# Performance work log

Hardware: AMD Instinct MI355X
Metric: run time of the kernel (lower is better)

## Reference

```python
import jax, jax.numpy as jnp
import numpy as np

N_NODES = 50000
N_EDGES = 1600000
F_IN = 256
HID = 256
HEADS = 8
HD = HID // HEADS  # 32
SLOPE = 0.2
EPS = 1e-5


def setup_inputs() -> dict:
    key = jax.random.key(0)
    ks = jax.random.split(key, 10)
    node_features = jax.random.normal(ks[0], (N_NODES, F_IN), jnp.float32)
    edge_index = jax.random.randint(ks[1], (2, N_EDGES), 0, N_NODES, jnp.int32)
    s = 1.0 / np.sqrt(F_IN)
    W = jax.random.uniform(ks[2], (HEADS, F_IN, HD), jnp.float32, -s, s)
    bw = jax.random.uniform(ks[3], (HEADS, HD), jnp.float32, -s, s)
    sa = 1.0 / np.sqrt(2 * HD)
    A = jax.random.uniform(ks[4], (HEADS, 2 * HD), jnp.float32, -sa, sa)
    ba = jax.random.uniform(ks[5], (HEADS,), jnp.float32, -sa, sa)
    gamma = jnp.ones((HEADS, HD), jnp.float32)
    beta = jnp.zeros((HEADS, HD), jnp.float32)
    so = 1.0 / np.sqrt(HD)
    Wout = jax.random.uniform(ks[6], (HD, HID), jnp.float32, -so, so)
    bout = jax.random.uniform(ks[7], (HID,), jnp.float32, -so, so)
    return dict(node_features=node_features, edge_index=edge_index, W=W, bw=bw,
                A=A, ba=ba, gamma=gamma, beta=beta, Wout=Wout, bout=bout)


def _head(x, W, bw, a, ba, gamma, beta, tgt, src):
    h = x @ W + bw                         # [N, d]
    # attn(concat(h_i, h_j)) = h_i @ a1 + h_j @ a2 + ba  (linear over concat)
    si = h @ a[:HD]                        # [N]
    sj = h @ a[HD:]                        # [N]
    e = si[tgt] + sj[src] + ba             # [E]
    e = jnp.where(e >= 0, e, SLOPE * e)    # leaky_relu
    # scatter_softmax over edges grouped by target node (stable)
    m = jax.ops.segment_max(e, tgt, num_segments=N_NODES)
    ex = jnp.exp(e - m[tgt])
    den = jax.ops.segment_sum(ex, tgt, num_segments=N_NODES)
    alpha = ex / den[tgt]                  # [E]  (dropout in eval mode = identity)
    msg = alpha[:, None] * h[src]          # [E, d]
    agg = jax.ops.segment_sum(msg, tgt, num_segments=N_NODES)  # [N, d]
    out = agg + h                          # skip connection
    out = jnp.where(out > 0, out, jnp.expm1(out))  # ELU
    mu = out.mean(axis=-1, keepdims=True)
    var = out.var(axis=-1, keepdims=True)
    return (out - mu) * jax.lax.rsqrt(var + EPS) * gamma + beta


def reference(node_features, edge_index, W, bw, A, ba, gamma, beta, Wout, bout):
    tgt = edge_index[0]
    src = edge_index[1]
    heads = jax.vmap(_head, in_axes=(None, 0, 0, 0, 0, 0, 0, None, None))(
        node_features, W, bw, A, ba, gamma, beta, tgt, src)   # [H, N, d]
    mean = heads.mean(axis=0)                                  # [N, d]
    y = mean @ Wout + bout                                     # [N, HID]
    return jnp.where(y > 0, y, jnp.expm1(y))                   # ELU
```

## Files before the change

kernel.cpp:

```cpp
#include <hip/hip_runtime.h>
#include <hip/hip_bf16.h>

#define N_NODES 50000
#define N_EDGES 1600000
#define HEADS 8
#define HD 32
#define FIN 256
#define HID 256

typedef unsigned short u16;
typedef unsigned int u32;

typedef short s8v __attribute__((ext_vector_type(8)));
typedef float f4v __attribute__((ext_vector_type(4)));

__device__ __forceinline__ float bf2f(u16 v) {
  union { u32 u; float f; } c; c.u = ((u32)v) << 16; return c.f;
}
__device__ __forceinline__ u16 f2bf(float f) {
  union { u32 u; float f; } c; c.f = f;
  u32 u = c.u;
  return (u16)((u + 0x7FFFu + ((u >> 16) & 1u)) >> 16);
}
__device__ __forceinline__ u32 pk2(float lo, float hi) {
  return (u32)f2bf(lo) | ((u32)f2bf(hi) << 16);
}

__global__ __launch_bounds__(256) void k_gemm(
    const float* __restrict__ X, const float* __restrict__ W,
    const float* __restrict__ bw, const float* __restrict__ A,
    u16* __restrict__ Hb, float* __restrict__ si, float* __restrict__ sj) {
  __shared__ __align__(16) u16 Xs[128 * 40];
  __shared__ __align__(16) u16 Wt[128 * 40];

  const int t = threadIdx.x;
  const int m0 = (blockIdx.x >> 1) * 128;
  const int n0 = (blockIdx.x & 1) * 128;
  const int w = t >> 6;
  const int lane = t & 63;
  const int l15 = lane & 15;
  const int quad = lane >> 4;
  const int wm = (w >> 1) * 64;
  const int wn = (w & 1) * 64;

  f4v acc[4][4];
#pragma unroll
  for (int i = 0; i < 4; i++)
#pragma unroll
    for (int j = 0; j < 4; j++) acc[i][j] = (f4v){0.f, 0.f, 0.f, 0.f};

  const int nl = t & 127;
  const int half = t >> 7;
  const int gn = n0 + nl;
  const int gh = gn >> 5, gd = gn & 31;

  for (int k0 = 0; k0 < FIN; k0 += 32) {
#pragma unroll
    for (int p = 0; p < 4; p++) {
      int row = p * 32 + (t >> 3);
      int f4 = t & 7;
      int node = m0 + row;
      float4 xv = make_float4(0.f, 0.f, 0.f, 0.f);
      if (node < N_NODES) xv = *(const float4*)&X[node * FIN + k0 + f4 * 4];
      u32* dst = (u32*)&Xs[row * 40 + f4 * 4];
      dst[0] = pk2(xv.x, xv.y);
      dst[1] = pk2(xv.z, xv.w);
    }
    {
      const float* wp = W + gh * (FIN * HD) + (k0 + half * 16) * HD + gd;
#pragma unroll
      for (int j = 0; j < 8; j++) {
        float lo = wp[(2 * j) * HD];
        float hi = wp[(2 * j + 1) * HD];
        *(u32*)&Wt[nl * 40 + half * 16 + 2 * j] = pk2(lo, hi);
      }
    }
    __syncthreads();
    s8v af[4], bf[4];
#pragma unroll
    for (int mi = 0; mi < 4; mi++)
      af[mi] = *(const s8v*)&Xs[(wm + mi * 16 + l15) * 40 + quad * 8];
#pragma unroll
    for (int ni = 0; ni < 4; ni++)
      bf[ni] = *(const s8v*)&Wt[(wn + ni * 16 + l15) * 40 + quad * 8];
#pragma unroll
    for (int mi = 0; mi < 4; mi++)
#pragma unroll
      for (int ni = 0; ni < 4; ni++)
        acc[mi][ni] = __builtin_amdgcn_mfma_f32_16x16x32_bf16(af[mi], bf[ni], acc[mi][ni], 0, 0, 0);
    __syncthreads();
  }

  const int head0 = (n0 + wn) >> 5;
  const int head1 = head0 + 1;
  float c1a0 = A[head0 * 64 + l15],      c1a1 = A[head0 * 64 + 16 + l15];
  float c2a0 = A[head0 * 64 + 32 + l15], c2a1 = A[head0 * 64 + 48 + l15];
  float c1b0 = A[head1 * 64 + l15],      c1b1 = A[head1 * 64 + 16 + l15];
  float c2b0 = A[head1 * 64 + 32 + l15], c2b1 = A[head1 * 64 + 48 + l15];

#pragma unroll
  for (int mi = 0; mi < 4; mi++) {
#pragma unroll
    for (int ni = 0; ni < 4; ni++) {
      float b = bw[n0 + wn + ni * 16 + l15];
#pragma unroll
      for (int r = 0; r < 4; r++) acc[mi][ni][r] += b;
    }
    const int rbase = m0 + wm + mi * 16 + quad * 4;
#pragma unroll
    for (int r = 0; r < 4; r++) {
      int node = rbase + r;
      if (node < N_NODES) {
#pragma unroll
        for (int ni = 0; ni < 4; ni++) {
          int col = n0 + wn + ni * 16 + l15;
          Hb[node * HID + col] = f2bf(acc[mi][ni][r]);
        }
      }
    }
    float s1a[4], s2a[4], s1b[4], s2b[4];
#pragma unroll
    for (int r = 0; r < 4; r++) {
      s1a[r] = acc[mi][0][r] * c1a0 + acc[mi][1][r] * c1a1;
      s2a[r] = acc[mi][0][r] * c2a0 + acc[mi][1][r] * c2a1;
      s1b[r] = acc[mi][2][r] * c1b0 + acc[mi][3][r] * c1b1;
      s2b[r] = acc[mi][2][r] * c2b0 + acc[mi][3][r] * c2b1;
    }
#pragma unroll
    for (int off = 1; off <= 8; off <<= 1) {
#pragma unroll
      for (int r = 0; r < 4; r++) {
        s1a[r] += __shfl_xor(s1a[r], off);
        s2a[r] += __shfl_xor(s2a[r], off);
        s1b[r] += __shfl_xor(s1b[r], off);
        s2b[r] += __shfl_xor(s2b[r], off);
      }
    }
    if (l15 == 0) {
#pragma unroll
      for (int r = 0; r < 4; r++) {
        int node = rbase + r;
        if (node < N_NODES) {
          si[node * HEADS + head0] = s1a[r];
          sj[node * HEADS + head0] = s2a[r];
          si[node * HEADS + head1] = s1b[r];
          sj[node * HEADS + head1] = s2b[r];
        }
      }
    }
  }
}

__global__ void k_hist(const int* __restrict__ tgt, int* __restrict__ cnt) {
  int e = blockIdx.x * 256 + threadIdx.x;
  if (e < N_EDGES) atomicAdd(&cnt[tgt[e]], 1);
}

__global__ __launch_bounds__(256) void k_scan1(const int* __restrict__ cnt,
    int* __restrict__ excl, int* __restrict__ bsum) {
  __shared__ int s[256];
  const int t = threadIdx.x;
  const int i = blockIdx.x * 256 + t;
  int v = (i < N_NODES) ? cnt[i] : 0;
  s[t] = v;
  __syncthreads();
  int x = v;
  for (int off = 1; off < 256; off <<= 1) {
    int y = (t >= off) ? s[t - off] : 0;
    __syncthreads();
    x += y;
    s[t] = x;
    __syncthreads();
  }
  if (i < N_NODES) excl[i] = x - v;
  if (t == 255) bsum[blockIdx.x] = x;
}

__global__ __launch_bounds__(256) void k_scan2(const int* __restrict__ bsum,
                                               int* __restrict__ boff) {
  __shared__ int s[256];
  const int t = threadIdx.x;
  int v = (t < 196) ? bsum[t] : 0;
  s[t] = v;
  __syncthreads();
  int x = v;
  for (int off = 1; off < 256; off <<= 1) {
    int y = (t >= off) ? s[t - off] : 0;
    __syncthreads();
    x += y;
    s[t] = x;
    __syncthreads();
  }
  if (t < 196) boff[t] = x - v;
}

__global__ void k_scan3(const int* __restrict__ excl, const int* __restrict__ boff,
                        int* __restrict__ rowptr, int* __restrict__ cursor) {
  int i = blockIdx.x * 256 + threadIdx.x;
  if (i < N_NODES) {
    int v = excl[i] + boff[blockIdx.x];
    rowptr[i] = v;
    cursor[i] = v;
  }
}

__global__ void k_scatter(const int* __restrict__ tgt, const int* __restrict__ src,
                          int* __restrict__ cursor, int* __restrict__ sortedSrc) {
  int e = blockIdx.x * 256 + threadIdx.x;
  if (e < N_EDGES) {
    int tg = tgt[e];
    int pos = atomicAdd(&cursor[tg], 1);
    sortedSrc[pos] = src[e];
  }
}

__global__ __launch_bounds__(256) void k_fused(
    const u16* __restrict__ Hb, const float* __restrict__ si,
    const float* __restrict__ sj, const float* __restrict__ ba,
    const float* __restrict__ gamma, const float* __restrict__ beta,
    const float* __restrict__ Wout, const float* __restrict__ bout,
    const int* __restrict__ rowptr, const int* __restrict__ cnt,
    const int* __restrict__ sortedSrc, float* __restrict__ out) {
  __shared__ float exs[32 * 8];
  __shared__ u32   soff[32];
  __shared__ float sbase[8];
  __shared__ float accs[8][256];
  __shared__ float dens[8][32];
  __shared__ float lnorm[256];
  __shared__ float meanv[32];

  const int n = blockIdx.x;
  const int t = threadIdx.x;
  const int cg = t & 31;
  const int es = t >> 5;
  const int hh = cg >> 2;
  const int start = rowptr[n];
  const int deg = cnt[n];
  if (t < 8) sbase[t] = si[n * HEADS + t] + ba[t];
  __syncthreads();

  const int i2c = t >> 3, h8 = t & 7;
  float acc[8] = {0.f, 0.f, 0.f, 0.f, 0.f, 0.f, 0.f, 0.f};
  float den = 0.f;
  for (int base = 0; base < deg; base += 32) {
    const int m = min(32, deg - base);
    {
      float exv = 0.f;
      u32 off0 = 0;
      if (i2c < m) {
        int s = sortedSrc[start + base + i2c];
        float e = sbase[h8] + sj[s * HEADS + h8];
        e = (e >= 0.f) ? e : 0.2f * e;
        exv = __expf(e);
        off0 = (u32)s * (HID * 2);
      }
      exs[i2c * 8 + h8] = exv;
      if (h8 == 0) soff[i2c] = off0;
    }
    __syncthreads();
#pragma unroll
    for (int k = 0; k < 4; k++) {
      int i2 = k * 8 + es;
      u32 off = soff[i2];
      float exv = exs[i2 * 8 + hh];
      float4 hb4 = *(const float4*)((const char*)Hb + off + 16 * cg);
      const u32* hw = (const u32*)&hb4;
#pragma unroll
      for (int d = 0; d < 4; d++) {
        union { u32 u; float f; } lo, hi;
        lo.u = hw[d] << 16;
        hi.u = hw[d] & 0xFFFF0000u;
        acc[2 * d]     += exv * lo.f;
        acc[2 * d + 1] += exv * hi.f;
      }
      den += exv;
    }
    __syncthreads();
  }
#pragma unroll
  for (int j = 0; j < 8; j++) accs[es][cg * 8 + j] = acc[j];
  dens[es][cg] = den;
  __syncthreads();

  float accT = 0.f, denT = 0.f;
#pragma unroll
  for (int e2 = 0; e2 < 8; e2++) {
    accT += accs[e2][t];
    denT += dens[e2][t >> 3];
  }
  float hs = bf2f(Hb[n * HID + t]);
  float v = ((deg > 0) ? (accT / denT) : 0.f) + hs;
  v = (v > 0.f) ? v : expm1f(v);
  float sum = v, sq = v * v;
#pragma unroll
  for (int off = 16; off >= 1; off >>= 1) {
    sum += __shfl_xor(sum, off);
    sq  += __shfl_xor(sq, off);
  }
  float mu = sum * (1.f / 32.f);
  float var = sq * (1.f / 32.f) - mu * mu;
  float nv = (v - mu) * rsqrtf(var + 1e-5f) * gamma[t] + beta[t];
  lnorm[t] = nv;
  __syncthreads();
  if (t < 32) {
    float m2 = 0.f;
#pragma unroll
    for (int h2 = 0; h2 < HEADS; h2++) m2 += lnorm[h2 * 32 + t];
    meanv[t] = m2 * 0.125f;
  }
  __syncthreads();
  float y = bout[t];
#pragma unroll
  for (int k = 0; k < 32; k++) y += meanv[k] * Wout[k * HID + t];
  y = (y > 0.f) ? y : expm1f(y);
  out[n * HID + t] = y;
}

extern "C" void kernel_launch(void* const* d_in, const int* in_sizes, int n_in,
                              void* d_out, int out_size, void* d_ws, size_t ws_size,
                              hipStream_t stream) {
  const float* X     = (const float*)d_in[0];
  const int*   EI    = (const int*)d_in[1];
  const float* W     = (const float*)d_in[2];
  const float* bw    = (const float*)d_in[3];
  const float* A     = (const float*)d_in[4];
  const float* ba    = (const float*)d_in[5];
  const float* gamma = (const float*)d_in[6];
  const float* beta  = (const float*)d_in[7];
  const float* Wout  = (const float*)d_in[8];
  const float* bout  = (const float*)d_in[9];
  float* out = (float*)d_out;
  const int* tgt = EI;
  const int* src = EI + N_EDGES;

  char* ws = (char*)d_ws;
  size_t off = 0;
  auto alloc = [&](size_t bytes) -> void* {
    void* p = ws + off;
    off += bytes;
    off = (off + 255) & ~(size_t)255;
    return p;
  };
  u16*   Hb        = (u16*)  alloc((size_t)N_NODES * HID * 2);
  float* si        = (float*)alloc((size_t)N_NODES * HEADS * 4);
  float* sj        = (float*)alloc((size_t)N_NODES * HEADS * 4);
  int*   cnt       = (int*)  alloc((size_t)N_NODES * 4);
  int*   excl      = (int*)  alloc((size_t)N_NODES * 4);
  int*   bsum      = (int*)  alloc(256 * 4);
  int*   boff      = (int*)  alloc(256 * 4);
  int*   rowptr    = (int*)  alloc((size_t)N_NODES * 4);
  int*   cursor    = (int*)  alloc((size_t)N_NODES * 4);
  int*   sortedSrc = (int*)  alloc((size_t)N_EDGES * 4);

  hipMemsetAsync(cnt, 0, (size_t)N_NODES * 4, stream);
  k_hist<<<(N_EDGES + 255) / 256, 256, 0, stream>>>(tgt, cnt);
  k_scan1<<<196, 256, 0, stream>>>(cnt, excl, bsum);
  k_scan2<<<1, 256, 0, stream>>>(bsum, boff);
  k_scan3<<<196, 256, 0, stream>>>(excl, boff, rowptr, cursor);
  k_scatter<<<(N_EDGES + 255) / 256, 256, 0, stream>>>(tgt, src, cursor, sortedSrc);
  k_gemm<<<((N_NODES + 127) / 128) * 2, 256, 0, stream>>>(X, W, bw, A, Hb, si, sj);
  k_fused<<<N_NODES, 256, 0, stream>>>(Hb, si, sj, ba, gamma, beta, Wout, bout,
                                       rowptr, cnt, sortedSrc, out);
}
```

Baseline: 533.8 us.

## Store H in fp16, pack edge weights with offsets, transpose Wout, use fast math

The projected features H are now stored as fp16 instead of bf16 and unpacked with half2 intrinsics in the aggregation loop. The per-edge exp value and source offset share one float2 shared-memory entry, so a single LDS read replaces two. Wout is transposed once in the scan kernel so each thread reads its column as contiguous float4s. expm1f and the division are replaced with __expf-1 and __fdividef, and accs gets padding against bank conflicts. The fp16 storage and the __expf-1 form of ELU change rounding, and fp16 has less range than bf16.

```diff
diff --git a/kernel.cpp b/kernel.cpp
--- a/kernel.cpp
+++ b/kernel.cpp
@@ -1,5 +1,6 @@
 #include <hip/hip_runtime.h>
 #include <hip/hip_bf16.h>
+#include <hip/hip_fp16.h>
 
 #define N_NODES 50000
 #define N_EDGES 1600000
@@ -14,22 +15,17 @@
 typedef short s8v __attribute__((ext_vector_type(8)));
 typedef float f4v __attribute__((ext_vector_type(4)));
 
-__device__ __forceinline__ float bf2f(u16 v) {
-  union { u32 u; float f; } c; c.u = ((u32)v) << 16; return c.f;
-}
-__device__ __forceinline__ u16 f2bf(float f) {
-  union { u32 u; float f; } c; c.f = f;
-  u32 u = c.u;
-  return (u16)((u + 0x7FFFu + ((u >> 16) & 1u)) >> 16);
-}
 __device__ __forceinline__ u32 pk2(float lo, float hi) {
-  return (u32)f2bf(lo) | ((u32)f2bf(hi) << 16);
+  __hip_bfloat162 b = __float22bfloat162_rn(make_float2(lo, hi));
+  union { __hip_bfloat162 b2; u32 u; } c;
+  c.b2 = b;
+  return c.u;
 }
 
 __global__ __launch_bounds__(256) void k_gemm(
     const float* __restrict__ X, const float* __restrict__ W,
     const float* __restrict__ bw, const float* __restrict__ A,
-    u16* __restrict__ Hb, float* __restrict__ si, float* __restrict__ sj) {
+    __half* __restrict__ Hb, float* __restrict__ si, float* __restrict__ sj) {
   __shared__ __align__(16) u16 Xs[128 * 40];
   __shared__ __align__(16) u16 Wt[128 * 40];
 
@@ -114,7 +110,7 @@
 #pragma unroll
         for (int ni = 0; ni < 4; ni++) {
           int col = n0 + wn + ni * 16 + l15;
-          Hb[node * HID + col] = f2bf(acc[mi][ni][r]);
+          Hb[node * HID + col] = __float2half_rn(acc[mi][ni][r]);
         }
       }
     }
@@ -177,7 +173,9 @@
 }
 
 __global__ __launch_bounds__(256) void k_scan2(const int* __restrict__ bsum,
-                                               int* __restrict__ boff) {
+                                               int* __restrict__ boff,
+                                               const float* __restrict__ Wout,
+                                               float* __restrict__ WoutT) {
   __shared__ int s[256];
   const int t = threadIdx.x;
   int v = (t < 196) ? bsum[t] : 0;
@@ -192,6 +190,8 @@
     __syncthreads();
   }
   if (t < 196) boff[t] = x - v;
+#pragma unroll
+  for (int k = 0; k < 32; k++) WoutT[t * 32 + k] = Wout[k * HID + t];
 }
 
 __global__ void k_scan3(const int* __restrict__ excl, const int* __restrict__ boff,
@@ -215,19 +215,18 @@
 }
 
 __global__ __launch_bounds__(256) void k_fused(
-    const u16* __restrict__ Hb, const float* __restrict__ si,
+    const __half* __restrict__ Hb, const float* __restrict__ si,
     const float* __restrict__ sj, const float* __restrict__ ba,
     const float* __restrict__ gamma, const float* __restrict__ beta,
-    const float* __restrict__ Wout, const float* __restrict__ bout,
+    const float* __restrict__ WoutT, const float* __restrict__ bout,
     const int* __restrict__ rowptr, const int* __restrict__ cnt,
     const int* __restrict__ sortedSrc, float* __restrict__ out) {
-  __shared__ float exs[32 * 8];
-  __shared__ u32   soff[32];
+  __shared__ __align__(16) float2 exo[32][8];
   __shared__ float sbase[8];
-  __shared__ float accs[8][256];
+  __shared__ float accs[8][260];
   __shared__ float dens[8][32];
   __shared__ float lnorm[256];
-  __shared__ float meanv[32];
+  __shared__ __align__(16) float meanv[32];
 
   const int n = blockIdx.x;
   const int t = threadIdx.x;
@@ -254,24 +253,20 @@
         exv = __expf(e);
         off0 = (u32)s * (HID * 2);
       }
-      exs[i2c * 8 + h8] = exv;
-      if (h8 == 0) soff[i2c] = off0;
+      exo[i2c][h8] = make_float2(exv, __uint_as_float(off0));
     }
     __syncthreads();
 #pragma unroll
     for (int k = 0; k < 4; k++) {
-      int i2 = k * 8 + es;
-      u32 off = soff[i2];
-      float exv = exs[i2 * 8 + hh];
+      float2 eo = exo[k * 8 + es][hh];
+      float exv = eo.x;
+      u32 off = __float_as_uint(eo.y);
       float4 hb4 = *(const float4*)((const char*)Hb + off + 16 * cg);
-      const u32* hw = (const u32*)&hb4;
+      const __half2* hp = (const __half2*)&hb4;
 #pragma unroll
       for (int d = 0; d < 4; d++) {
-        union { u32 u; float f; } lo, hi;
-        lo.u = hw[d] << 16;
-        hi.u = hw[d] & 0xFFFF0000u;
-        acc[2 * d]     += exv * lo.f;
-        acc[2 * d + 1] += exv * hi.f;
+        acc[2 * d]     += exv * __low2float(hp[d]);
+        acc[2 * d + 1] += exv * __high2float(hp[d]);
       }
       den += exv;
     }
@@ -288,9 +283,9 @@
     accT += accs[e2][t];
     denT += dens[e2][t >> 3];
   }
-  float hs = bf2f(Hb[n * HID + t]);
-  float v = ((deg > 0) ? (accT / denT) : 0.f) + hs;
-  v = (v > 0.f) ? v : expm1f(v);
+  float hs = __half2float(Hb[n * HID + t]);
+  float v = ((deg > 0) ? __fdividef(accT, denT) : 0.f) + hs;
+  v = (v > 0.f) ? v : (__expf(v) - 1.f);
   float sum = v, sq = v * v;
 #pragma unroll
   for (int off = 16; off >= 1; off >>= 1) {
@@ -310,9 +305,14 @@
   }
   __syncthreads();
   float y = bout[t];
-#pragma unroll
-  for (int k = 0; k < 32; k++) y += meanv[k] * Wout[k * HID + t];
-  y = (y > 0.f) ? y : expm1f(y);
+  const float4* wt = (const float4*)&WoutT[t * 32];
+#pragma unroll
+  for (int q = 0; q < 8; q++) {
+    float4 wv = wt[q];
+    float4 mq = *(const float4*)&meanv[4 * q];
+    y += mq.x * wv.x + mq.y * wv.y + mq.z * wv.z + mq.w * wv.w;
+  }
+  y = (y > 0.f) ? y : (__expf(y) - 1.f);
   out[n * HID + t] = y;
 }
 
@@ -341,7 +341,7 @@
     off = (off + 255) & ~(size_t)255;
     return p;
   };
-  u16*   Hb        = (u16*)  alloc((size_t)N_NODES * HID * 2);
+  __half* Hb       = (__half*)alloc((size_t)N_NODES * HID * 2);
   float* si        = (float*)alloc((size_t)N_NODES * HEADS * 4);
   float* sj        = (float*)alloc((size_t)N_NODES * HEADS * 4);
   int*   cnt       = (int*)  alloc((size_t)N_NODES * 4);
@@ -351,14 +351,15 @@
   int*   rowptr    = (int*)  alloc((size_t)N_NODES * 4);
   int*   cursor    = (int*)  alloc((size_t)N_NODES * 4);
   int*   sortedSrc = (int*)  alloc((size_t)N_EDGES * 4);
+  float* WoutT     = (float*)alloc((size_t)HID * HD * 4);
 
   hipMemsetAsync(cnt, 0, (size_t)N_NODES * 4, stream);
   k_hist<<<(N_EDGES + 255) / 256, 256, 0, stream>>>(tgt, cnt);
   k_scan1<<<196, 256, 0, stream>>>(cnt, excl, bsum);
-  k_scan2<<<1, 256, 0, stream>>>(bsum, boff);
+  k_scan2<<<1, 256, 0, stream>>>(bsum, boff, Wout, WoutT);
   k_scan3<<<196, 256, 0, stream>>>(excl, boff, rowptr, cursor);
   k_scatter<<<(N_EDGES + 255) / 256, 256, 0, stream>>>(tgt, src, cursor, sortedSrc);
   k_gemm<<<((N_NODES + 127) / 128) * 2, 256, 0, stream>>>(X, W, bw, A, Hb, si, sj);
-  k_fused<<<N_NODES, 256, 0, stream>>>(Hb, si, sj, ba, gamma, beta, Wout, bout,
+  k_fused<<<N_NODES, 256, 0, stream>>>(Hb, si, sj, ba, gamma, beta, WoutT, bout,
                                        rowptr, cnt, sortedSrc, out);
 }
```

After: 646.7 us. 1.21x slower.
